# Optimization experiments

Hardware: AMD Instinct MI355X
Metric: run time of the kernel (lower is better)

## Reference

```python
import jax, jax.numpy as jnp
import numpy as np

B, J, C = 8, 2048, 256
K = 32
H = 8
D = 32  # out_dim per head


def setup_inputs() -> dict:
    key = jax.random.key(0)
    k0, k1, k2, k3, k4, k5 = jax.random.split(key, 6)
    x = jax.random.normal(k0, (B, J, C), dtype=jnp.float32)
    nbr_idx = jax.random.randint(k1, (B, J, K), 0, J)
    s_in = 1.0 / np.sqrt(C)
    s_hd = 1.0 / np.sqrt(H * D)
    Wq = jax.random.uniform(k2, (C, H * D), dtype=jnp.float32, minval=-s_in, maxval=s_in)
    Wk = jax.random.uniform(k3, (C, H * D), dtype=jnp.float32, minval=-s_in, maxval=s_in)
    Wv = jax.random.uniform(k4, (C, H * D), dtype=jnp.float32, minval=-s_in, maxval=s_in)
    Wp = jax.random.uniform(k5, (H * D, D), dtype=jnp.float32, minval=-s_hd, maxval=s_hd)
    return {"x": x, "nbr_idx": nbr_idx, "Wq": Wq, "Wk": Wk, "Wv": Wv, "Wp": Wp}


def reference(x, nbr_idx, Wq, Wk, Wv, Wp):
    b, j, c = x.shape
    q = (x @ Wq).reshape(b, j, H, D)  # [B,J,H,D]
    k = (x @ Wk).reshape(b, j, H, D)
    v = (x @ Wv).reshape(b, j, H, D)
    bidx = jnp.arange(b)[:, None, None]  # [B,1,1]
    k_nbr = k[bidx, nbr_idx]  # [B,J,K,H,D]
    v_nbr = v[bidx, nbr_idx]  # [B,J,K,H,D]
    attn = jnp.einsum("bjhd,bjkhd->bjkh", q, k_nbr) / np.sqrt(D)
    attn = jax.nn.leaky_relu(attn, negative_slope=0.2)
    attn = jax.nn.softmax(attn, axis=2)  # softmax over K neighbors
    out = jnp.einsum("bjkh,bjkhd->bjhd", attn, v_nbr).reshape(b, j, H * D)
    return out @ Wp  # [B,J,D]
```

## Files before the change

kernel.cpp:

```cpp
#include <hip/hip_runtime.h>
#include <hip/hip_bf16.h>


typedef short bf16x8 __attribute__((ext_vector_type(8)));
typedef float f32x4  __attribute__((ext_vector_type(4)));
typedef float f32x2  __attribute__((ext_vector_type(2)));

__device__ __forceinline__ float bf2f(unsigned short u) {
    union { unsigned int i; float f; } c; c.i = ((unsigned int)u) << 16; return c.f;
}
__device__ __forceinline__ unsigned short f2bf(float f) {
    union { float f; unsigned int i; } c; c.f = f;
    unsigned int r = c.i + 0x7FFFu + ((c.i >> 16) & 1u);
    return (unsigned short)(r >> 16);
}
__device__ __forceinline__ f32x2 upk(unsigned int u) {
    union { unsigned int i; float f; } lo, hi;
    lo.i = u << 16;
    hi.i = u & 0xffff0000u;
    return (f32x2){lo.f, hi.f};
}

__device__ __forceinline__ void gld_lds16(void* lds, const void* g) {
    __builtin_amdgcn_global_load_lds(
        (const __attribute__((address_space(1))) unsigned int*)g,
        (__attribute__((address_space(3))) unsigned int*)lds,
        16, 0, 0);
}

__global__ __launch_bounds__(256) void prep(
    const float* __restrict__ x,
    const float* __restrict__ Wq, const float* __restrict__ Wk,
    const float* __restrict__ Wv, const float* __restrict__ Wp,
    unsigned short* __restrict__ xb, unsigned short* __restrict__ Wt)
{
    const int blk = blockIdx.x, tid = threadIdx.x;
    if (blk < 4096) {
        int t = blk * 256 + tid;
        float4 f = ((const float4*)x)[t];
        ushort4 u;
        u.x = f2bf(f.x); u.y = f2bf(f.y); u.z = f2bf(f.z); u.w = f2bf(f.w);
        ((ushort4*)xb)[t] = u;
        return;
    }
    int wi = blk - 4096;
    int w = wi >> 8, n = wi & 255, t = tid;
    if (w == 0) {
        Wt[(size_t)n * 256 + t] = f2bf(Wq[(size_t)t * 256 + n]);
    } else if (w == 1) {
        Wt[(size_t)(256 + n) * 256 + t] = f2bf(Wk[(size_t)t * 256 + n]);
    } else {
        int h = n >> 5, c = n & 31;
        float acc = 0.f;
#pragma unroll
        for (int d = 0; d < 32; d++)
            acc += Wv[(size_t)t * 256 + h * 32 + d] * Wp[(size_t)(h * 32 + d) * 32 + c];
        Wt[(size_t)(512 + n) * 256 + t] = f2bf(acc);
    }
}

__global__ __launch_bounds__(256) void qkv_mfma(
    const unsigned short* __restrict__ xb,
    const unsigned short* __restrict__ Wt,
    unsigned short* __restrict__ Q, unsigned short* __restrict__ Kp,
    unsigned short* __restrict__ VP)
{
    __shared__ unsigned short Als[128][64];
    __shared__ unsigned short Bls[128][64];

    const unsigned short* Wb = Wt + (size_t)blockIdx.z * 65536;
    unsigned short* Y = (blockIdx.z == 0) ? Q : (blockIdx.z == 1) ? Kp : VP;

    const int row0 = blockIdx.x * 128;
    const int col0 = blockIdx.y * 128;
    const int tid  = threadIdx.x;
    const int w    = tid >> 6, l = tid & 63;
    const int wm   = (w >> 1) * 64, wn = (w & 1) * 64;
    const int lm   = l & 15, quad = l >> 4;

    f32x4 acc[4][4];
#pragma unroll
    for (int i = 0; i < 4; i++)
#pragma unroll
        for (int j = 0; j < 4; j++) acc[i][j] = (f32x4){0.f, 0.f, 0.f, 0.f};

    const char* Ab = (const char*)(xb + (size_t)row0 * 256);
    const char* Bb = (const char*)(Wb + (size_t)col0 * 256);

    for (int k0 = 0; k0 < 256; k0 += 64) {
#pragma unroll
        for (int i = 0; i < 4; i++) {
            int s = i * 256 + tid;
            int r = s >> 3, c = s & 7;
            size_t go = (size_t)r * 512 + (size_t)k0 * 2 + c * 16;
            gld_lds16((char*)Als + s * 16, Ab + go);
            gld_lds16((char*)Bls + s * 16, Bb + go);
        }
        __syncthreads();

#pragma unroll
        for (int kk = 0; kk < 64; kk += 32) {
            bf16x8 a[4], b[4];
#pragma unroll
            for (int tm = 0; tm < 4; tm++)
                a[tm] = *(const bf16x8*)&Als[wm + tm * 16 + lm][kk + quad * 8];
#pragma unroll
            for (int tn = 0; tn < 4; tn++)
                b[tn] = *(const bf16x8*)&Bls[wn + tn * 16 + lm][kk + quad * 8];
#pragma unroll
            for (int tm = 0; tm < 4; tm++)
#pragma unroll
                for (int tn = 0; tn < 4; tn++)
                    acc[tm][tn] = __builtin_amdgcn_mfma_f32_16x16x32_bf16(
                        a[tm], b[tn], acc[tm][tn], 0, 0, 0);
        }
        __syncthreads();
    }

#pragma unroll
    for (int tm = 0; tm < 4; tm++) {
        int rbase = row0 + wm + tm * 16 + quad * 4;
#pragma unroll
        for (int tn = 0; tn < 4; tn++) {
            int col = col0 + wn + tn * 16 + lm;
#pragma unroll
            for (int r = 0; r < 4; r++)
                Y[(size_t)(rbase + r) * 256 + col] = f2bf(acc[tm][tn][r]);
        }
    }
}

__global__ __launch_bounds__(256) void attn_all(
    const unsigned short* __restrict__ qb,
    const unsigned short* __restrict__ kb,
    const unsigned short* __restrict__ vp,
    const int*            __restrict__ nbr,
    float*                __restrict__ out)
{
    __shared__ float sc[8 * 33];
    __shared__ float pw[8 * 33];
    __shared__ float redB[8 * 264];
    __shared__ float red2[256];

    const int b   = blockIdx.x & 7;
    const int j   = blockIdx.x >> 3;
    const int bj  = (b << 11) + j;
    const int tid = threadIdx.x;

    const int w    = tid >> 6;
    const int l    = tid & 63;
    const int lh   = l & 31;
    const int half = l >> 5;
    const int hA   = lh >> 2;
    const int g    = 2 * w + half;
    const size_t bbase = (size_t)b << 19;
    const int* nrow = nbr + (size_t)bj * 32;

    uint4 qu = *(const uint4*)(qb + (size_t)bj * 256 + lh * 8);

    int koA[4], koB[4];
#pragma unroll
    for (int p = 0; p < 4; p++) koA[p] = nrow[w * 8 + 2 * p + half] << 8;
#pragma unroll
    for (int p = 0; p < 4; p++) koB[p] = nrow[p * 8 + g] << 8;

    uint4 ku[4], vu[4];
#pragma unroll
    for (int p = 0; p < 4; p++)
        ku[p] = *(const uint4*)(kb + bbase + koA[p] + lh * 8);
#pragma unroll
    for (int p = 0; p < 4; p++)
        vu[p] = *(const uint4*)(vp + bbase + koB[p] + lh * 8);

    f32x2 qf[4];
    qf[0] = upk(qu.x); qf[1] = upk(qu.y); qf[2] = upk(qu.z); qf[3] = upk(qu.w);

#pragma unroll
    for (int p = 0; p < 4; p++) {
        const int kkA = w * 8 + 2 * p + half;
        f32x2 a2 = (f32x2){0.f, 0.f};
        a2 += upk(ku[p].x) * qf[0];
        a2 += upk(ku[p].y) * qf[1];
        a2 += upk(ku[p].z) * qf[2];
        a2 += upk(ku[p].w) * qf[3];
        float acc = a2.x + a2.y;
        acc += __shfl_xor(acc, 1);
        acc += __shfl_xor(acc, 2);
        if ((l & 3) == 0) {
            float s = acc * 0.17677669529663687f;
            s = (s > 0.f) ? s : 0.2f * s;
            sc[hA * 33 + kkA] = s;
        }
    }
    __syncthreads();

    {
        const int h2  = 2 * w + half;
        const int kk2 = lh;
        float s = sc[h2 * 33 + kk2];
        float mx = s;
#pragma unroll
        for (int m = 16; m >= 1; m >>= 1) mx = fmaxf(mx, __shfl_xor(mx, m));
        float e = __expf(s - mx);
        float sum = e;
#pragma unroll
        for (int m = 16; m >= 1; m >>= 1) sum += __shfl_xor(sum, m);
        pw[h2 * 33 + kk2] = e / sum;
    }
    __syncthreads();

    {
        f32x2 a0 = (f32x2){0.f,0.f}, a1 = a0, a2v = a0, a3 = a0;
#pragma unroll
        for (int p = 0; p < 4; p++) {
            const int kkB = p * 8 + g;
            const float wgt = pw[hA * 33 + kkB];
            const f32x2 w2 = (f32x2){wgt, wgt};
            a0  += upk(vu[p].x) * w2;
            a1  += upk(vu[p].y) * w2;
            a2v += upk(vu[p].z) * w2;
            a3  += upk(vu[p].w) * w2;
        }
        float* rb = &redB[g * 264 + lh * 8];
        *(float4*)(rb)     = make_float4(a0.x, a0.y, a1.x, a1.y);
        *(float4*)(rb + 4) = make_float4(a2v.x, a2v.y, a3.x, a3.y);
    }
    __syncthreads();

    {
        float s = 0.f;
#pragma unroll
        for (int gg = 0; gg < 8; gg++) s += redB[gg * 264 + tid];
        red2[tid] = s;
    }
    __syncthreads();

    if (tid < 32) {
        float o = 0.f;
#pragma unroll
        for (int h = 0; h < 8; h++) o += red2[h * 32 + tid];
        out[(size_t)bj * 32 + tid] = o;
    }
}

__global__ __launch_bounds__(256) void fused_all(
    const float* __restrict__ X, const int* __restrict__ nbr,
    const float* __restrict__ Wq, const float* __restrict__ Wk,
    const float* __restrict__ Wv, const float* __restrict__ Wp,
    float* __restrict__ out)
{
    __shared__ float xr[256], qrow[256], xn[256];
    __shared__ float vn[32][256];
    __shared__ int   nb[32];
    __shared__ float sc[32][8], pwv[32][8];
    __shared__ float sp[256], hd[256];
    __shared__ float red[8][32];

    const int bj = blockIdx.x, b = bj >> 11, tid = threadIdx.x;

    xr[tid] = X[(size_t)bj * 256 + tid];
    if (tid < 32) nb[tid] = nbr[(size_t)bj * 32 + tid];
    __syncthreads();

    {
        float acc = 0.f;
#pragma unroll 8
        for (int c = 0; c < 256; c++) acc += xr[c] * Wq[(size_t)c * 256 + tid];
        qrow[tid] = acc;
    }
    __syncthreads();

    for (int i = 0; i < 32; i++) {
        size_t r = (size_t)(b * 2048 + nb[i]);
        xn[tid] = X[r * 256 + tid];
        __syncthreads();
        float ka = 0.f, va = 0.f;
#pragma unroll 8
        for (int c = 0; c < 256; c++) {
            float xc = xn[c];
            ka += xc * Wk[(size_t)c * 256 + tid];
            va += xc * Wv[(size_t)c * 256 + tid];
        }
        vn[i][tid] = va;
        sp[tid] = qrow[tid] * ka;
        __syncthreads();
        if (tid < 8) {
            float s = 0.f;
#pragma unroll
            for (int d = 0; d < 32; d++) s += sp[tid * 32 + d];
            s *= 0.17677669529663687f;
            s = (s > 0.f) ? s : 0.2f * s;
            sc[i][tid] = s;
        }
        __syncthreads();
    }

    {
        const int h = tid & 7, kk = tid >> 3;
        float mx = -1e30f;
#pragma unroll
        for (int i = 0; i < 32; i++) mx = fmaxf(mx, sc[i][h]);
        float ssum = 0.f;
#pragma unroll
        for (int i = 0; i < 32; i++) ssum += __expf(sc[i][h] - mx);
        pwv[kk][h] = __expf(sc[kk][h] - mx) / ssum;
    }
    __syncthreads();

    {
        const int h2 = tid >> 5;
        float acc = 0.f;
#pragma unroll 8
        for (int i = 0; i < 32; i++) acc += pwv[i][h2] * vn[i][tid];
        hd[tid] = acc;
    }
    __syncthreads();

    {
        const int c = tid & 31, ch = tid >> 5;
        float p = 0.f;
#pragma unroll
        for (int i = 0; i < 32; i++) { int r = ch * 32 + i; p += hd[r] * Wp[r * 32 + c]; }
        red[ch][c] = p;
    }
    __syncthreads();

    if (tid < 32) {
        float o = 0.f;
#pragma unroll
        for (int i = 0; i < 8; i++) o += red[i][tid];
        out[(size_t)bj * 32 + tid] = o;
    }
}

extern "C" void kernel_launch(void* const* d_in, const int* in_sizes, int n_in,
                              void* d_out, int out_size, void* d_ws, size_t ws_size,
                              hipStream_t stream) {
    const float* x   = (const float*)d_in[0];
    const int*   nbr = (const int*)d_in[1];
    const float* Wq  = (const float*)d_in[2];
    const float* Wk  = (const float*)d_in[3];
    const float* Wv  = (const float*)d_in[4];
    const float* Wp  = (const float*)d_in[5];
    float*       out = (float*)d_out;

    const size_t ME   = (size_t)16384 * 256;
    const size_t need = (4 * ME + 3 * 65536) * sizeof(unsigned short);

    if (ws_size >= need) {
        unsigned short* q  = (unsigned short*)d_ws;
        unsigned short* k  = q + ME;
        unsigned short* vp = k + ME;
        unsigned short* xb = vp + ME;
        unsigned short* Wt = xb + ME;

        prep<<<4096 + 768, 256, 0, stream>>>(x, Wq, Wk, Wv, Wp, xb, Wt);
        qkv_mfma<<<dim3(128, 2, 3), 256, 0, stream>>>(xb, Wt, q, k, vp);
        attn_all<<<16384, 256, 0, stream>>>(q, k, vp, nbr, out);
    } else {
        fused_all<<<16384, 256, 0, stream>>>(x, nbr, Wq, Wk, Wv, Wp, out);
    }
}
```

Before: 124.6 us.

## Map one query per wavefront in attention kernel, dropping shared memory and barriers

The attention kernel is restructured so that each 64-lane wavefront handles one (b,j) query rather than one query per 256-thread block. Neighbor offsets are broadcast with shuffles, the scores and softmax stay in registers, and the final head/neighbor reduction uses xor shuffles. This removes all LDS traffic and __syncthreads barriers and cuts the launch to a quarter as many blocks. In exchange each lane does more sequential gather work and holds more registers, and the K and V loads are serialized into batches of four instead of all being issued up front.

Result: slower. 134.1 us (+7.6%).

```diff
diff --git a/kernel.cpp b/kernel.cpp
--- a/kernel.cpp
+++ b/kernel.cpp
@@ -137,109 +137,100 @@
     const int*            __restrict__ nbr,
     float*                __restrict__ out)
 {
-    __shared__ float sc[8 * 33];
-    __shared__ float pw[8 * 33];
-    __shared__ float redB[8 * 264];
-    __shared__ float red2[256];
-
-    const int b   = blockIdx.x & 7;
-    const int j   = blockIdx.x >> 3;
-    const int bj  = (b << 11) + j;
-    const int tid = threadIdx.x;
-
-    const int w    = tid >> 6;
-    const int l    = tid & 63;
+    const int wv = threadIdx.x >> 6;
+    const int l  = threadIdx.x & 63;
+    const int qi = blockIdx.x * 4 + wv;
+    const int b  = qi & 7;
+    const int j  = qi >> 3;
+    const int bj = (b << 11) + j;
+
     const int lh   = l & 31;
     const int half = l >> 5;
-    const int hA   = lh >> 2;
-    const int g    = 2 * w + half;
     const size_t bbase = (size_t)b << 19;
-    const int* nrow = nbr + (size_t)bj * 32;
 
     uint4 qu = *(const uint4*)(qb + (size_t)bj * 256 + lh * 8);
-
-    int koA[4], koB[4];
-#pragma unroll
-    for (int p = 0; p < 4; p++) koA[p] = nrow[w * 8 + 2 * p + half] << 8;
-#pragma unroll
-    for (int p = 0; p < 4; p++) koB[p] = nrow[p * 8 + g] << 8;
-
-    uint4 ku[4], vu[4];
-#pragma unroll
-    for (int p = 0; p < 4; p++)
-        ku[p] = *(const uint4*)(kb + bbase + koA[p] + lh * 8);
-#pragma unroll
-    for (int p = 0; p < 4; p++)
-        vu[p] = *(const uint4*)(vp + bbase + koB[p] + lh * 8);
+    int ko = nbr[(size_t)bj * 32 + lh] << 8;
 
     f32x2 qf[4];
     qf[0] = upk(qu.x); qf[1] = upk(qu.y); qf[2] = upk(qu.z); qf[3] = upk(qu.w);
 
-#pragma unroll
-    for (int p = 0; p < 4; p++) {
-        const int kkA = w * 8 + 2 * p + half;
-        f32x2 a2 = (f32x2){0.f, 0.f};
-        a2 += upk(ku[p].x) * qf[0];
-        a2 += upk(ku[p].y) * qf[1];
-        a2 += upk(ku[p].z) * qf[2];
-        a2 += upk(ku[p].w) * qf[3];
-        float acc = a2.x + a2.y;
-        acc += __shfl_xor(acc, 1);
-        acc += __shfl_xor(acc, 2);
-        if ((l & 3) == 0) {
+    float sreg[16];
+#pragma unroll
+    for (int pb = 0; pb < 4; pb++) {
+        uint4 u[4];
+#pragma unroll
+        for (int i = 0; i < 4; i++) {
+            const int p = pb * 4 + i;
+            const int kof = __shfl(ko, 2 * p + half);
+            u[i] = *(const uint4*)(kb + bbase + kof + lh * 8);
+        }
+#pragma unroll
+        for (int i = 0; i < 4; i++) {
+            const int p = pb * 4 + i;
+            f32x2 a2 = (f32x2){0.f, 0.f};
+            a2 += upk(u[i].x) * qf[0];
+            a2 += upk(u[i].y) * qf[1];
+            a2 += upk(u[i].z) * qf[2];
+            a2 += upk(u[i].w) * qf[3];
+            float acc = a2.x + a2.y;
+            acc += __shfl_xor(acc, 1);
+            acc += __shfl_xor(acc, 2);
             float s = acc * 0.17677669529663687f;
-            s = (s > 0.f) ? s : 0.2f * s;
-            sc[hA * 33 + kkA] = s;
-        }
-    }
-    __syncthreads();
-
-    {
-        const int h2  = 2 * w + half;
-        const int kk2 = lh;
-        float s = sc[h2 * 33 + kk2];
-        float mx = s;
-#pragma unroll
-        for (int m = 16; m >= 1; m >>= 1) mx = fmaxf(mx, __shfl_xor(mx, m));
-        float e = __expf(s - mx);
-        float sum = e;
-#pragma unroll
-        for (int m = 16; m >= 1; m >>= 1) sum += __shfl_xor(sum, m);
-        pw[h2 * 33 + kk2] = e / sum;
-    }
-    __syncthreads();
-
-    {
-        f32x2 a0 = (f32x2){0.f,0.f}, a1 = a0, a2v = a0, a3 = a0;
-#pragma unroll
-        for (int p = 0; p < 4; p++) {
-            const int kkB = p * 8 + g;
-            const float wgt = pw[hA * 33 + kkB];
-            const f32x2 w2 = (f32x2){wgt, wgt};
-            a0  += upk(vu[p].x) * w2;
-            a1  += upk(vu[p].y) * w2;
-            a2v += upk(vu[p].z) * w2;
-            a3  += upk(vu[p].w) * w2;
-        }
-        float* rb = &redB[g * 264 + lh * 8];
-        *(float4*)(rb)     = make_float4(a0.x, a0.y, a1.x, a1.y);
-        *(float4*)(rb + 4) = make_float4(a2v.x, a2v.y, a3.x, a3.y);
-    }
-    __syncthreads();
-
-    {
-        float s = 0.f;
-#pragma unroll
-        for (int gg = 0; gg < 8; gg++) s += redB[gg * 264 + tid];
-        red2[tid] = s;
-    }
-    __syncthreads();
-
-    if (tid < 32) {
-        float o = 0.f;
-#pragma unroll
-        for (int h = 0; h < 8; h++) o += red2[h * 32 + tid];
-        out[(size_t)bj * 32 + tid] = o;
+            sreg[p] = (s > 0.f) ? s : 0.2f * s;
+        }
+    }
+
+    float mx = sreg[0];
+#pragma unroll
+    for (int i = 1; i < 16; i++) mx = fmaxf(mx, sreg[i]);
+    mx = fmaxf(mx, __shfl_xor(mx, 32));
+    float sum = 0.f;
+    float pwreg[16];
+#pragma unroll
+    for (int i = 0; i < 16; i++) { pwreg[i] = __expf(sreg[i] - mx); sum += pwreg[i]; }
+    sum += __shfl_xor(sum, 32);
+    const float inv = 1.0f / sum;
+#pragma unroll
+    for (int i = 0; i < 16; i++) pwreg[i] *= inv;
+
+    f32x2 acc[4];
+#pragma unroll
+    for (int i = 0; i < 4; i++) acc[i] = (f32x2){0.f, 0.f};
+#pragma unroll
+    for (int pb = 0; pb < 4; pb++) {
+        uint4 u[4];
+#pragma unroll
+        for (int i = 0; i < 4; i++) {
+            const int p = pb * 4 + i;
+            const int kof = __shfl(ko, 2 * p + half);
+            u[i] = *(const uint4*)(vp + bbase + kof + lh * 8);
+        }
+#pragma unroll
+        for (int i = 0; i < 4; i++) {
+            const int p = pb * 4 + i;
+            const f32x2 w2 = (f32x2){pwreg[p], pwreg[p]};
+            acc[0] += upk(u[i].x) * w2;
+            acc[1] += upk(u[i].y) * w2;
+            acc[2] += upk(u[i].z) * w2;
+            acc[3] += upk(u[i].w) * w2;
+        }
+    }
+
+#pragma unroll
+    for (int m = 32; m >= 4; m >>= 1) {
+        if (m == 16 || m == 8 || m == 4 || m == 32) {
+#pragma unroll
+            for (int i = 0; i < 4; i++) {
+                acc[i].x += __shfl_xor(acc[i].x, m);
+                acc[i].y += __shfl_xor(acc[i].y, m);
+            }
+        }
+    }
+
+    if (l < 4) {
+        float* op = out + (size_t)bj * 32 + l * 8;
+        *(float4*)(op)     = make_float4(acc[0].x, acc[0].y, acc[1].x, acc[1].y);
+        *(float4*)(op + 4) = make_float4(acc[2].x, acc[2].y, acc[3].x, acc[3].y);
     }
 }
 
@@ -356,7 +347,7 @@
 
         prep<<<4096 + 768, 256, 0, stream>>>(x, Wq, Wk, Wv, Wp, xb, Wt);
         qkv_mfma<<<dim3(128, 2, 3), 256, 0, stream>>>(xb, Wt, q, k, vp);
-        attn_all<<<16384, 256, 0, stream>>>(q, k, vp, nbr, out);
+        attn_all<<<4096, 256, 0, stream>>>(q, k, vp, nbr, out);
     } else {
         fused_all<<<16384, 256, 0, stream>>>(x, nbr, Wq, Wk, Wv, Wp, out);
     }
```
